# Performance work log

Measured on AMD Instinct MI355X. Metric: run time of the kernel, lower is better.

Reference implementation:

```python
import jax, jax.numpy as jnp
import numpy as np

S = 128          # spatial grid size per axis
N = 100000       # active voxels
C_IN = 32
C_OUT = 32
FS = 3           # filter size per axis -> 27 offsets


def _build_rulebook():
    """Build submanifold-conv rulebook: for each active site and each of the
    27 filter offsets, the index of the active neighbor (or masked out)."""
    rng = np.random.default_rng(0)
    coords = rng.integers(0, S, size=(2 * N, 3))
    lin = coords[:, 0] * S * S + coords[:, 1] * S + coords[:, 2]
    lin = np.unique(lin)[:N]                      # sorted unique active sites
    xyz = np.stack([lin // (S * S), (lin // S) % S, lin % S], axis=1)  # [N,3]
    offs = np.stack(np.meshgrid(*([np.arange(FS) - FS // 2] * 3), indexing='ij'), -1).reshape(-1, 3)  # [27,3]
    nb = xyz[:, None, :] + offs[None, :, :]       # [N,27,3]
    inb = np.all((nb >= 0) & (nb < S), axis=-1)   # in-bounds
    nb_lin = nb[..., 0] * S * S + nb[..., 1] * S + nb[..., 2]
    pos = np.searchsorted(lin, nb_lin)
    pos_c = np.clip(pos, 0, N - 1)
    found = inb & (lin[pos_c] == nb_lin)
    nbr_idx = np.where(found, pos_c, 0).astype(np.int32)   # [N,27]
    return nbr_idx, found


def setup_inputs() -> dict:
    key = jax.random.key(0)
    k1, k2 = jax.random.split(key)
    nbr_idx, nbr_mask = _build_rulebook()
    K = FS ** 3
    std = (2.0 / C_IN / K) ** 0.5   # matches module init
    return {
        'features': jax.random.normal(k1, (N, C_IN), dtype=jnp.float32),
        'weight': std * jax.random.normal(k2, (K, C_IN, C_OUT), dtype=jnp.float32),
        'bias': jnp.zeros((C_OUT,), dtype=jnp.float32),
        'nbr_idx': jnp.asarray(nbr_idx),
        'nbr_mask': jnp.asarray(nbr_mask),
    }


def reference(features, weight, bias, nbr_idx, nbr_mask):
    # Submanifold sparse conv: gather active neighbors per filter offset,
    # multiply by per-offset [Cin,Cout] weight, accumulate at active sites.
    gathered = jnp.where(nbr_mask[:, :, None], features[nbr_idx], 0.0)  # [N,K,Cin]
    out = jnp.einsum('nki,kio->no', gathered, weight) + bias            # [N,Cout]
    return out
```

## Files before the change

kernel.cpp:

```cpp
#include <hip/hip_runtime.h>
#include <hip/hip_bf16.h>

#define NVOX 100000
#define CIN 32
#define COUT 32
#define KOFF 27

typedef __attribute__((ext_vector_type(8))) short short8;
typedef __attribute__((ext_vector_type(4))) float float4v;
typedef __attribute__((ext_vector_type(4))) int   int4v;

__device__ __forceinline__ short f2bf(float x) {
    union { float f; unsigned u; } v; v.f = x;
    unsigned u = v.u;
    u += 0x7FFFu + ((u >> 16) & 1u);
    return (short)(u >> 16);
}

__global__ __launch_bounds__(256) void feat_cvt_kernel(
    const float* __restrict__ feat, unsigned short* __restrict__ fbf)
{
    int i = (blockIdx.x * 256 + threadIdx.x) * 4;
    if (i >= NVOX * CIN) return;
    float4v f = *(const float4v*)(feat + i);
    short s[4] = { f2bf(f.x), f2bf(f.y), f2bf(f.z), f2bf(f.w) };
    *(ulonglong1*)(fbf + i) = *(ulonglong1*)s;
}

__global__ __launch_bounds__(256) void wgt_cvt_kernel(
    const float* __restrict__ weight, short8* __restrict__ wfrag)
{
    int g = blockIdx.x * 256 + threadIdx.x;
    if (g >= KOFF * 2 * 64) return;
    int k   = g >> 7;
    int rem = g & 127;
    int t   = rem >> 6;
    int ln  = rem & 63;
    int co  = t * 16 + (ln & 15);
    int cib = (ln >> 4) * 8;
    const float* wp = weight + (k * CIN + cib) * COUT + co;
    short8 b;
#pragma unroll
    for (int j = 0; j < 8; ++j) b[j] = f2bf(wp[j * COUT]);
    wfrag[g] = b;
}

__global__ __launch_bounds__(512, 4) void subm_conv_kernel(
    const unsigned short* __restrict__ fbf,
    const short8* __restrict__ wfrag,
    const float* __restrict__ bias,
    const int* __restrict__ nbr_idx,
    const int* __restrict__ nbr_mask,
    float* __restrict__ out)
{
    __shared__ short8 wlds[KOFF * 2 * 64];

    const int tid = threadIdx.x;
    for (int g = tid; g < KOFF * 2 * 64; g += 512) wlds[g] = wfrag[g];
    __syncthreads();

    const int lane = tid & 63;
    const int wave = tid >> 6;
    const int m    = lane & 15;
    const int quad = lane >> 4;

    const int v0 = (blockIdx.x * 8 + wave) * 16;
    int v = v0 + m;
    if (v > NVOX - 1) v = NVOX - 1;
    const int base = v * KOFF;

    int enc[KOFF];
#pragma unroll
    for (int k = 0; k < KOFF; ++k) enc[k] = nbr_idx[base + k];
    int mok[KOFF];
#pragma unroll
    for (int k = 0; k < KOFF; ++k) mok[k] = nbr_mask[base + k];
#pragma unroll
    for (int k = 0; k < KOFF; ++k) enc[k] = mok[k] ? enc[k] : -1;

    float4v acc0 = {0.f, 0.f, 0.f, 0.f};
    float4v acc1 = {0.f, 0.f, 0.f, 0.f};

    const int cioff = quad * 8;

    short8 abuf[8];
#pragma unroll
    for (int k = 0; k < 8; ++k) {
        int row = enc[k] < 0 ? 0 : enc[k];
        abuf[k] = *(const short8*)(fbf + (size_t)row * CIN + cioff);
    }

#pragma unroll
    for (int k = 0; k < KOFF; ++k) {
        const int slot = k & 7;
        union { short8 s; int4v i; } a;
        a.s = abuf[slot];
        if (k + 8 < KOFF) {
            int row = enc[k + 8] < 0 ? 0 : enc[k + 8];
            abuf[slot] = *(const short8*)(fbf + (size_t)row * CIN + cioff);
        }
        int zmask = enc[k] >= 0 ? ~0 : 0;
        a.i &= int4v{zmask, zmask, zmask, zmask};

        short8 wb0 = wlds[k * 128 + lane];
        short8 wb1 = wlds[k * 128 + 64 + lane];
        acc0 = __builtin_amdgcn_mfma_f32_16x16x32_bf16(a.s, wb0, acc0, 0, 0, 0);
        acc1 = __builtin_amdgcn_mfma_f32_16x16x32_bf16(a.s, wb1, acc1, 0, 0, 0);
    }

    const float bs0 = bias[m];
    const float bs1 = bias[16 + m];
#pragma unroll
    for (int r = 0; r < 4; ++r) {
        int vv = v0 + quad * 4 + r;
        if (vv < NVOX) {
            out[(size_t)vv * COUT + m]      = acc0[r] + bs0;
            out[(size_t)vv * COUT + 16 + m] = acc1[r] + bs1;
        }
    }
}

extern "C" void kernel_launch(void* const* d_in, const int* in_sizes, int n_in,
                              void* d_out, int out_size, void* d_ws, size_t ws_size,
                              hipStream_t stream) {
    const float* feat = (const float*)d_in[0];
    const float* wgt  = (const float*)d_in[1];
    const float* bias = (const float*)d_in[2];
    const int*   nidx = (const int*)d_in[3];
    const int*   nmsk = (const int*)d_in[4];
    float*       out  = (float*)d_out;

    unsigned short* fbf   = (unsigned short*)d_ws;
    short8*         wfrag = (short8*)((char*)d_ws + (size_t)NVOX * CIN * 2);

    feat_cvt_kernel<<<(NVOX * CIN / 4 + 255) / 256, 256, 0, stream>>>(feat, fbf);
    wgt_cvt_kernel<<<(KOFF * 2 * 64 + 255) / 256, 256, 0, stream>>>(wgt, wfrag);

    const int block = 512;
    const int grid  = (NVOX + 127) / 128;
    subm_conv_kernel<<<grid, block, 0, stream>>>(fbf, wfrag, bias, nidx, nmsk, out);
}
```

Measured before the change: 104.2 us.

## Fold neighbor mask into index with zero sentinel row, enlarge blocks

After: 105.9 us. About the same (+1.6%).

```diff
diff --git a/kernel.cpp b/kernel.cpp
--- a/kernel.cpp
+++ b/kernel.cpp
@@ -21,10 +21,14 @@
     const float* __restrict__ feat, unsigned short* __restrict__ fbf)
 {
     int i = (blockIdx.x * 256 + threadIdx.x) * 4;
-    if (i >= NVOX * CIN) return;
-    float4v f = *(const float4v*)(feat + i);
-    short s[4] = { f2bf(f.x), f2bf(f.y), f2bf(f.z), f2bf(f.w) };
-    *(ulonglong1*)(fbf + i) = *(ulonglong1*)s;
+    if (i < NVOX * CIN) {
+        float4v f = *(const float4v*)(feat + i);
+        short s[4] = { f2bf(f.x), f2bf(f.y), f2bf(f.z), f2bf(f.w) };
+        *(ulonglong1*)(fbf + i) = *(ulonglong1*)s;
+    } else if (i < (NVOX + 1) * CIN) {
+        short s[4] = { 0, 0, 0, 0 };
+        *(ulonglong1*)(fbf + i) = *(ulonglong1*)s;
+    }
 }
 
 __global__ __launch_bounds__(256) void wgt_cvt_kernel(
@@ -45,67 +49,71 @@
     wfrag[g] = b;
 }
 
-__global__ __launch_bounds__(512, 4) void subm_conv_kernel(
+__global__ __launch_bounds__(256) void enc_fold_kernel(
+    const int* __restrict__ nbr_idx, const int* __restrict__ nbr_mask,
+    int* __restrict__ enc)
+{
+    int i = (blockIdx.x * 256 + threadIdx.x) * 4;
+    if (i >= NVOX * KOFF) return;
+    int4v id = *(const int4v*)(nbr_idx + i);
+    int4v mk = *(const int4v*)(nbr_mask + i);
+    int4v e;
+    e.x = mk.x ? id.x : NVOX;
+    e.y = mk.y ? id.y : NVOX;
+    e.z = mk.z ? id.z : NVOX;
+    e.w = mk.w ? id.w : NVOX;
+    *(int4v*)(enc + i) = e;
+}
+
+__global__ __launch_bounds__(1024, 8) void subm_conv_kernel(
     const unsigned short* __restrict__ fbf,
     const short8* __restrict__ wfrag,
     const float* __restrict__ bias,
-    const int* __restrict__ nbr_idx,
-    const int* __restrict__ nbr_mask,
+    const int* __restrict__ enc_g,
     float* __restrict__ out)
 {
     __shared__ short8 wlds[KOFF * 2 * 64];
 
-    const int tid = threadIdx.x;
-    for (int g = tid; g < KOFF * 2 * 64; g += 512) wlds[g] = wfrag[g];
-    __syncthreads();
-
+    const int tid  = threadIdx.x;
     const int lane = tid & 63;
     const int wave = tid >> 6;
     const int m    = lane & 15;
     const int quad = lane >> 4;
 
-    const int v0 = (blockIdx.x * 8 + wave) * 16;
+    const int v0 = (blockIdx.x * 16 + wave) * 16;
     int v = v0 + m;
     if (v > NVOX - 1) v = NVOX - 1;
-    const int base = v * KOFF;
 
+    const int* ep = enc_g + v * KOFF;
     int enc[KOFF];
 #pragma unroll
-    for (int k = 0; k < KOFF; ++k) enc[k] = nbr_idx[base + k];
-    int mok[KOFF];
-#pragma unroll
-    for (int k = 0; k < KOFF; ++k) mok[k] = nbr_mask[base + k];
-#pragma unroll
-    for (int k = 0; k < KOFF; ++k) enc[k] = mok[k] ? enc[k] : -1;
+    for (int k = 0; k < KOFF; ++k) enc[k] = ep[k];
+
+    for (int g = tid; g < KOFF * 2 * 64; g += 1024) wlds[g] = wfrag[g];
+    __syncthreads();
 
     float4v acc0 = {0.f, 0.f, 0.f, 0.f};
     float4v acc1 = {0.f, 0.f, 0.f, 0.f};
 
-    const int cioff = quad * 8;
+    const char* fb = (const char*)fbf;
+    const int   boff = quad * 16;
 
-    short8 abuf[8];
+    short8 abuf[4];
 #pragma unroll
-    for (int k = 0; k < 8; ++k) {
-        int row = enc[k] < 0 ? 0 : enc[k];
-        abuf[k] = *(const short8*)(fbf + (size_t)row * CIN + cioff);
-    }
+    for (int k = 0; k < 4; ++k)
+        abuf[k] = *(const short8*)(fb + (size_t)enc[k] * 64 + boff);
 
 #pragma unroll
     for (int k = 0; k < KOFF; ++k) {
-        const int slot = k & 7;
-        union { short8 s; int4v i; } a;
-        a.s = abuf[slot];
-        if (k + 8 < KOFF) {
-            int row = enc[k + 8] < 0 ? 0 : enc[k + 8];
-            abuf[slot] = *(const short8*)(fbf + (size_t)row * CIN + cioff);
-        }
-        int zmask = enc[k] >= 0 ? ~0 : 0;
-        a.i &= int4v{zmask, zmask, zmask, zmask};
+        const int slot = k & 3;
+        short8 a = abuf[slot];
+        if (k + 4 < KOFF)
+            abuf[slot] = *(const short8*)(fb + (size_t)enc[k + 4] * 64 + boff);
 
         short8 wb0 = wlds[k * 128 + lane];
         short8 wb1 = wlds[k * 128 + 64 + lane];
-        acc0 = __builtin_amdgcn_mfma_f32_16x16x32_bf16(a.s, wb0, acc0, 0, 0, 0);
-        acc1 = __builtin_amdgcn_mfma_f32_16x16x32_bf16(a.s, wb1, acc1, 0, 0, 0);
+        acc0 = __builtin_amdgcn_mfma_f32_16x16x32_bf16(a, wb0, acc0, 0, 0, 0);
+        acc1 = __builtin_amdgcn_mfma_f32_16x16x32_bf16(a, wb1, acc1, 0, 0, 0);
     }
 
     const float bs0 = bias[m];
@@ -131,12 +139,14 @@
     float*       out  = (float*)d_out;
 
     unsigned short* fbf   = (unsigned short*)d_ws;
-    short8*         wfrag = (short8*)((char*)d_ws + (size_t)NVOX * CIN * 2);
+    short8*         wfrag = (short8*)((char*)d_ws + 6400064);
+    int*            enc   = (int*)((char*)d_ws + 6400064 + 55296);
 
-    feat_cvt_kernel<<<(NVOX * CIN / 4 + 255) / 256, 256, 0, stream>>>(feat, fbf);
+    feat_cvt_kernel<<<((NVOX + 1) * CIN / 4 + 255) / 256, 256, 0, stream>>>(feat, fbf);
     wgt_cvt_kernel<<<(KOFF * 2 * 64 + 255) / 256, 256, 0, stream>>>(wgt, wfrag);
+    enc_fold_kernel<<<(NVOX * KOFF / 4 + 255) / 256, 256, 0, stream>>>(nidx, nmsk, enc);
 
-    const int block = 512;
-    const int grid  = (NVOX + 127) / 128;
-    subm_conv_kernel<<<grid, block, 0, stream>>>(fbf, wfrag, bias, nidx, nmsk, out);
+    const int block = 1024;
+    const int grid  = (NVOX + 255) / 256;
+    subm_conv_kernel<<<grid, block, 0, stream>>>(fbf, wfrag, bias, enc, out);
 }
```

## Merge conversion kernels, add zero row for masked neighbors, stage output through LDS

Applied to the files above, without the earlier changes.

New measurement: 99.19 us. -4.8%, faster.

```diff
diff --git a/kernel.cpp b/kernel.cpp
--- a/kernel.cpp
+++ b/kernel.cpp
@@ -5,10 +5,10 @@
 #define CIN 32
 #define COUT 32
 #define KOFF 27
+#define NTILE 6250
 
 typedef __attribute__((ext_vector_type(8))) short short8;
 typedef __attribute__((ext_vector_type(4))) float float4v;
-typedef __attribute__((ext_vector_type(4))) int   int4v;
 
 __device__ __forceinline__ short f2bf(float x) {
     union { float f; unsigned u; } v; v.f = x;
@@ -17,32 +17,37 @@
     return (short)(u >> 16);
 }
 
-__global__ __launch_bounds__(256) void feat_cvt_kernel(
-    const float* __restrict__ feat, unsigned short* __restrict__ fbf)
+#define FEAT_BLOCKS 3126
+
+__global__ __launch_bounds__(256) void cvt_kernel(
+    const float* __restrict__ feat, const float* __restrict__ weight,
+    unsigned short* __restrict__ fbf, short8* __restrict__ wfrag)
 {
-    int i = (blockIdx.x * 256 + threadIdx.x) * 4;
-    if (i >= NVOX * CIN) return;
-    float4v f = *(const float4v*)(feat + i);
-    short s[4] = { f2bf(f.x), f2bf(f.y), f2bf(f.z), f2bf(f.w) };
-    *(ulonglong1*)(fbf + i) = *(ulonglong1*)s;
-}
-
-__global__ __launch_bounds__(256) void wgt_cvt_kernel(
-    const float* __restrict__ weight, short8* __restrict__ wfrag)
-{
-    int g = blockIdx.x * 256 + threadIdx.x;
-    if (g >= KOFF * 2 * 64) return;
-    int k   = g >> 7;
-    int rem = g & 127;
-    int t   = rem >> 6;
-    int ln  = rem & 63;
-    int co  = t * 16 + (ln & 15);
-    int cib = (ln >> 4) * 8;
-    const float* wp = weight + (k * CIN + cib) * COUT + co;
-    short8 b;
+    if (blockIdx.x < FEAT_BLOCKS) {
+        int i = (blockIdx.x * 256 + threadIdx.x) * 4;
+        if (i < NVOX * CIN) {
+            float4v f = *(const float4v*)(feat + i);
+            short s[4] = { f2bf(f.x), f2bf(f.y), f2bf(f.z), f2bf(f.w) };
+            *(ulonglong1*)(fbf + i) = *(ulonglong1*)s;
+        } else if (i < (NVOX + 1) * CIN) {
+            short s[4] = { 0, 0, 0, 0 };
+            *(ulonglong1*)(fbf + i) = *(ulonglong1*)s;
+        }
+    } else {
+        int g = (blockIdx.x - FEAT_BLOCKS) * 256 + threadIdx.x;
+        if (g >= KOFF * 2 * 64) return;
+        int k   = g >> 7;
+        int rem = g & 127;
+        int t   = rem >> 6;
+        int ln  = rem & 63;
+        int co  = t * 16 + (ln & 15);
+        int cib = (ln >> 4) * 8;
+        const float* wp = weight + (k * CIN + cib) * COUT + co;
+        short8 b;
 #pragma unroll
-    for (int j = 0; j < 8; ++j) b[j] = f2bf(wp[j * COUT]);
-    wfrag[g] = b;
+        for (int j = 0; j < 8; ++j) b[j] = f2bf(wp[j * COUT]);
+        wfrag[g] = b;
+    }
 }
 
 __global__ __launch_bounds__(512, 4) void subm_conv_kernel(
@@ -55,16 +60,15 @@
 {
     __shared__ short8 wlds[KOFF * 2 * 64];
 
-    const int tid = threadIdx.x;
-    for (int g = tid; g < KOFF * 2 * 64; g += 512) wlds[g] = wfrag[g];
-    __syncthreads();
-
+    const int tid  = threadIdx.x;
     const int lane = tid & 63;
     const int wave = tid >> 6;
     const int m    = lane & 15;
     const int quad = lane >> 4;
+    const int tile = blockIdx.x * 8 + wave;
+    const bool tv  = tile < NTILE;
 
-    const int v0 = (blockIdx.x * 8 + wave) * 16;
+    const int v0 = tile * 16;
     int v = v0 + m;
     if (v > NVOX - 1) v = NVOX - 1;
     const int base = v * KOFF;
@@ -76,46 +80,53 @@
 #pragma unroll
     for (int k = 0; k < KOFF; ++k) mok[k] = nbr_mask[base + k];
 #pragma unroll
-    for (int k = 0; k < KOFF; ++k) enc[k] = mok[k] ? enc[k] : -1;
+    for (int k = 0; k < KOFF; ++k) enc[k] = (mok[k] ? enc[k] : NVOX) << 6;
+
+    for (int g = tid; g < KOFF * 2 * 64; g += 512) wlds[g] = wfrag[g];
+    __syncthreads();
 
     float4v acc0 = {0.f, 0.f, 0.f, 0.f};
     float4v acc1 = {0.f, 0.f, 0.f, 0.f};
 
-    const int cioff = quad * 8;
+    const char* fb   = (const char*)fbf;
+    const int   boff = quad * 16;
 
     short8 abuf[8];
 #pragma unroll
-    for (int k = 0; k < 8; ++k) {
-        int row = enc[k] < 0 ? 0 : enc[k];
-        abuf[k] = *(const short8*)(fbf + (size_t)row * CIN + cioff);
-    }
+    for (int k = 0; k < 8; ++k)
+        abuf[k] = *(const short8*)(fb + (size_t)(unsigned)enc[k] + boff);
 
 #pragma unroll
     for (int k = 0; k < KOFF; ++k) {
         const int slot = k & 7;
-        union { short8 s; int4v i; } a;
-        a.s = abuf[slot];
-        if (k + 8 < KOFF) {
-            int row = enc[k + 8] < 0 ? 0 : enc[k + 8];
-            abuf[slot] = *(const short8*)(fbf + (size_t)row * CIN + cioff);
-        }
-        int zmask = enc[k] >= 0 ? ~0 : 0;
-        a.i &= int4v{zmask, zmask, zmask, zmask};
+        short8 a = abuf[slot];
+        if (k + 8 < KOFF)
+            abuf[slot] = *(const short8*)(fb + (size_t)(unsigned)enc[k + 8] + boff);
 
         short8 wb0 = wlds[k * 128 + lane];
         short8 wb1 = wlds[k * 128 + 64 + lane];
-        acc0 = __builtin_amdgcn_mfma_f32_16x16x32_bf16(a.s, wb0, acc0, 0, 0, 0);
-        acc1 = __builtin_amdgcn_mfma_f32_16x16x32_bf16(a.s, wb1, acc1, 0, 0, 0);
+        acc0 = __builtin_amdgcn_mfma_f32_16x16x32_bf16(a, wb0, acc0, 0, 0, 0);
+        acc1 = __builtin_amdgcn_mfma_f32_16x16x32_bf16(a, wb1, acc1, 0, 0, 0);
     }
+
+    __syncthreads();
+    float* tb = (float*)wlds + wave * (16 * 36);
 
     const float bs0 = bias[m];
     const float bs1 = bias[16 + m];
+    if (tv) {
 #pragma unroll
-    for (int r = 0; r < 4; ++r) {
-        int vv = v0 + quad * 4 + r;
-        if (vv < NVOX) {
-            out[(size_t)vv * COUT + m]      = acc0[r] + bs0;
-            out[(size_t)vv * COUT + 16 + m] = acc1[r] + bs1;
+        for (int r = 0; r < 4; ++r) {
+            tb[(quad * 4 + r) * 36 + m]      = acc0[r] + bs0;
+            tb[(quad * 4 + r) * 36 + 16 + m] = acc1[r] + bs1;
+        }
+#pragma unroll
+        for (int p = 0; p < 2; ++p) {
+            int flat = p * 64 + lane;
+            int row  = flat >> 3;
+            int ch   = flat & 7;
+            float4v val = *(const float4v*)(tb + row * 36 + ch * 4);
+            *(float4v*)(out + (size_t)(v0 + row) * COUT + ch * 4) = val;
         }
     }
 }
@@ -130,13 +141,14 @@
     const int*   nmsk = (const int*)d_in[4];
     float*       out  = (float*)d_out;
 
-    unsigned short* fbf   = (unsigned short*)d_ws;
-    short8*         wfrag = (short8*)((char*)d_ws + (size_t)NVOX * CIN * 2);
+    char* ws = (char*)d_ws;
+    unsigned short* fbf   = (unsigned short*)ws;
+    short8*         wfrag = (short8*)(ws + 6400128);
 
-    feat_cvt_kernel<<<(NVOX * CIN / 4 + 255) / 256, 256, 0, stream>>>(feat, fbf);
-    wgt_cvt_kernel<<<(KOFF * 2 * 64 + 255) / 256, 256, 0, stream>>>(wgt, wfrag);
+    const int wgt_blocks = (KOFF * 2 * 64 + 255) / 256;
+    cvt_kernel<<<FEAT_BLOCKS + wgt_blocks, 256, 0, stream>>>(feat, wgt, fbf, wfrag);
 
     const int block = 512;
-    const int grid  = (NVOX + 127) / 128;
+    const int grid  = (NTILE + 7) / 8;
     subm_conv_kernel<<<grid, block, 0, stream>>>(fbf, wfrag, bias, nidx, nmsk, out);
 }
```
